# Kernel optimization log

Measured on AMD Instinct MI355X. Metric: run time of the kernel, lower is better.

## Reference

```python
import jax, jax.numpy as jnp
import numpy as np
import math

N_EMBD = 512
N_BRANCH = 4
BLOCK = 2048
B, T = 2, 2048


def make_rope_tables(dim, max_len):
    inv_freq = 1.0 / (10000.0 ** (np.arange(0, dim, 2, dtype=np.float32) / dim))
    t = np.arange(max_len, dtype=np.float32)
    freqs = np.einsum('i,j->ij', t, inv_freq)  # [max_len, dim/2]
    return jnp.asarray(np.cos(freqs)), jnp.asarray(np.sin(freqs))


def apply_rope(xq, cos, sin):
    # xq: [..., T, C]; cos/sin: [T, C/2]
    x1 = xq[..., 0::2]
    x2 = xq[..., 1::2]
    y1 = x1 * cos - x2 * sin
    y2 = x1 * sin + x2 * cos
    return jnp.stack((y1, y2), axis=-1).reshape(xq.shape)


def setup_inputs() -> dict:
    key = jax.random.key(0)
    ks = jax.random.split(key, 6)
    C, NB = N_EMBD, N_BRANCH
    s = 1.0 / math.sqrt(C)
    a = jax.random.normal(ks[0], (B, T, C), jnp.float32)
    x = jax.random.normal(ks[1], (B, T, C), jnp.float32)
    Wq = jax.random.normal(ks[2], (C, C * NB), jnp.float32) * s
    Wk = jax.random.normal(ks[3], (C, C), jnp.float32) * s
    Wv = jax.random.normal(ks[4], (C, C * NB), jnp.float32) * s
    Wo = jax.random.normal(ks[5], (C, C), jnp.float32) * s
    cos, sin = make_rope_tables(C, BLOCK)
    return {"a": a, "x": x, "Wq": Wq, "Wk": Wk, "Wv": Wv, "Wo": Wo,
            "cos": cos, "sin": sin}


def reference(a, x, Wq, Wk, Wv, Wo, cos, sin):
    Bb, Tt, C = x.shape
    NB = Wq.shape[1] // C
    cos_t = cos[:Tt]
    sin_t = sin[:Tt]

    q = (a @ Wq).reshape(Bb, Tt, NB, C).transpose(0, 2, 1, 3)  # [B,NB,T,C]
    v = (a @ Wv).reshape(Bb, Tt, NB, C).transpose(0, 2, 1, 3)  # [B,NB,T,C]
    k = (x @ Wk)[:, None, :, :]                                # [B,1,T,C]

    q = apply_rope(q, cos_t, sin_t)
    k = apply_rope(k, cos_t, sin_t)

    att = jnp.einsum('bntc,bosc->bnts', q, k) / math.sqrt(C)   # [B,NB,T,T]
    causal = jnp.tril(jnp.ones((Tt, Tt), bool))                # [T,T]
    att_m = jnp.where(causal, att, -jnp.inf)

    # softmax over branch axis; mask is identical across branches, so compute
    # on unmasked logits and zero-out masked positions (== nan_to_num of
    # softmax over fully -inf columns)
    soft_probs = jnp.where(causal, jax.nn.softmax(att, axis=1), 0.0)

    max_val = jnp.max(soft_probs, axis=1, keepdims=True)
    hard_mask = jax.lax.stop_gradient((soft_probs == max_val).astype(att.dtype))
    route_mask = jax.lax.stop_gradient(hard_mask - soft_probs) + soft_probs

    att_max = jnp.max(att_m, axis=1)                           # [B,T,T]
    attn_probs = jax.nn.softmax(att_max, axis=-1)              # [B,T,T]

    combined = attn_probs[:, None, :, :] * route_mask          # [B,NB,T,T]
    y = jnp.einsum('bnts,bnsc->btc', combined, v)              # [B,T,C]
    return y @ Wo
```

## Files before the change

### kernel.cpp

```cpp
#include <hip/hip_runtime.h>
#include <math.h>


#define B_ 2
#define T_ 2048
#define C_ 512
#define NB_ 4
#define C2_ 1024

typedef unsigned short u16;
typedef unsigned char u8;
using short8 = __attribute__((ext_vector_type(8))) short;
using bf16x8 = __attribute__((ext_vector_type(8))) __bf16;
using f32x4  = __attribute__((ext_vector_type(4))) float;

__device__ __forceinline__ float bf2f(u16 u) {
  union { unsigned int i; float f; } v; v.i = ((unsigned int)u) << 16; return v.f;
}
__device__ __forceinline__ u16 f2bf(float f) {
  union { float f; unsigned int i; } v; v.f = f;
  unsigned int u = v.i;
  return (u16)((u + 0x7fffu + ((u >> 16) & 1u)) >> 16);
}
__device__ __forceinline__ f32x4 mfma16x16x32(short8 a, short8 b, f32x4 c) {
  return __builtin_amdgcn_mfma_f32_16x16x32_bf16(
      __builtin_bit_cast(bf16x8, a), __builtin_bit_cast(bf16x8, b), c, 0, 0, 0);
}
__device__ __forceinline__ void split8(const float* s, uint4& hi, uint4& lo) {
  u16 h[8], l[8];
#pragma unroll
  for (int j = 0; j < 8; ++j) {
    h[j] = f2bf(s[j]);
    l[j] = f2bf(s[j] - bf2f(h[j]));
  }
  hi.x = h[0] | ((unsigned)h[1] << 16); hi.y = h[2] | ((unsigned)h[3] << 16);
  hi.z = h[4] | ((unsigned)h[5] << 16); hi.w = h[6] | ((unsigned)h[7] << 16);
  lo.x = l[0] | ((unsigned)l[1] << 16); lo.y = l[2] | ((unsigned)l[3] << 16);
  lo.z = l[4] | ((unsigned)l[5] << 16); lo.w = l[6] | ((unsigned)l[7] << 16);
}
__device__ __forceinline__ int swz(int row) { return ((row >> 1) & 3) << 3; }

template <int MODE>
__global__ __launch_bounds__(256) void gemm_qk(const float* __restrict__ A,
                                               const float* __restrict__ W,
                                               u16* __restrict__ out,
                                               const float* __restrict__ cosT,
                                               const float* __restrict__ sinT,
                                               const int N, const int K) {
  __shared__ u16 Ah[64][32], Al[64][32];
  __shared__ u16 Bh[64][32], Bl[64][32];
  const int tid = threadIdx.x;
  const int wave = tid >> 6, lane = tid & 63;
  const int m0 = blockIdx.y << 6, n0 = blockIdx.x << 6;
  const f32x4 zero = {0.f, 0.f, 0.f, 0.f};
  f32x4 acc[4] = {zero, zero, zero, zero};
  const int srow = tid >> 2, koff = ((tid & 3) << 3) ^ swz(tid >> 2);
  const int lrow = lane & 15, lk = ((lane >> 4) << 3) ^ swz(lane & 15);
  for (int kk = 0; kk < K; kk += 32) {
    const int kg = (tid & 3) << 3;
    float av[8];
    *(float4*)(av) = *(const float4*)(&A[(size_t)(m0 + srow) * K + kk + kg]);
    *(float4*)(av + 4) =
        *(const float4*)(&A[(size_t)(m0 + srow) * K + kk + kg + 4]);
    uint4 hi, lo;
    split8(av, hi, lo);
    *(uint4*)(&Ah[srow][koff]) = hi;
    *(uint4*)(&Al[srow][koff]) = lo;
    float wv[8];
#pragma unroll
    for (int j = 0; j < 8; ++j)
      wv[j] = W[(size_t)(kk + kg + j) * N + n0 + srow];
    split8(wv, hi, lo);
    *(uint4*)(&Bh[srow][koff]) = hi;
    *(uint4*)(&Bl[srow][koff]) = lo;
    __syncthreads();
    short8 ah = *(const short8*)(&Ah[(wave << 4) + lrow][lk]);
    short8 al = *(const short8*)(&Al[(wave << 4) + lrow][lk]);
#pragma unroll
    for (int ns = 0; ns < 4; ++ns) {
      short8 bh = *(const short8*)(&Bh[(ns << 4) + lrow][lk]);
      short8 bl = *(const short8*)(&Bl[(ns << 4) + lrow][lk]);
      acc[ns] = mfma16x16x32(ah, bh, acc[ns]);
      acc[ns] = mfma16x16x32(al, bh, acc[ns]);
      acc[ns] = mfma16x16x32(ah, bl, acc[ns]);
    }
    __syncthreads();
  }
  const int r0 = m0 + (wave << 4) + ((lane >> 4) << 2);
  const int cb = n0 + (lane & 15);
#pragma unroll
  for (int ns = 0; ns < 4; ++ns) {
#pragma unroll
    for (int r = 0; r < 4; ++r) {
      const int rg = r0 + r;
      const int cg = cb + (ns << 4);
      float v = acc[ns][r];
      float pv = __shfl_xor(v, 1);
      const int t = rg & (T_ - 1);
      const int c = (MODE == 1) ? (cg & (C_ - 1)) : cg;
      const int i = c >> 1;
      const float cf = cosT[(t << 8) + i];
      const float sf = sinT[(t << 8) + i];
      float x1 = (lane & 1) ? pv : v;
      float x2 = (lane & 1) ? v : pv;
      float y = (lane & 1) ? (x1 * sf + x2 * cf) : (x1 * cf - x2 * sf);
      if (MODE == 1) y *= 0.044194173824159216f;
      const u16 hi = f2bf(y);
      const u16 lo = f2bf(y - bf2f(hi));
      size_t rowoff;
      if (MODE == 1) {
        const int b = rg >> 11, n = cg >> 9;
        rowoff = ((size_t)((b * NB_ + n) * T_ + t)) * C2_;
      } else {
        rowoff = (size_t)rg * C2_;
      }
      out[rowoff + c] = hi;
      out[rowoff + C_ + c] = lo;
    }
  }
}

template <int AF32, int OF32>
__global__ __launch_bounds__(256) void gemm_hi(const void* __restrict__ Ap,
                                               const float* __restrict__ W,
                                               void* __restrict__ outp,
                                               const int N, const int K) {
  __shared__ u16 As[64][32];
  __shared__ u16 Bs[64][32];
  const int tid = threadIdx.x;
  const int wave = tid >> 6, lane = tid & 63;
  const int m0 = blockIdx.y << 6, n0 = blockIdx.x << 6;
  const f32x4 zero = {0.f, 0.f, 0.f, 0.f};
  f32x4 acc[4] = {zero, zero, zero, zero};
  const int srow = tid >> 2, koff = ((tid & 3) << 3) ^ swz(tid >> 2);
  const int lrow = lane & 15, lk = ((lane >> 4) << 3) ^ swz(lane & 15);
  for (int kk = 0; kk < K; kk += 32) {
    const int kg = (tid & 3) << 3;
    if (AF32) {
      const float* A = (const float*)Ap;
      float av[8];
      *(float4*)(av) = *(const float4*)(&A[(size_t)(m0 + srow) * K + kk + kg]);
      *(float4*)(av + 4) =
          *(const float4*)(&A[(size_t)(m0 + srow) * K + kk + kg + 4]);
      uint4 hi;
      hi.x = f2bf(av[0]) | ((unsigned)f2bf(av[1]) << 16);
      hi.y = f2bf(av[2]) | ((unsigned)f2bf(av[3]) << 16);
      hi.z = f2bf(av[4]) | ((unsigned)f2bf(av[5]) << 16);
      hi.w = f2bf(av[6]) | ((unsigned)f2bf(av[7]) << 16);
      *(uint4*)(&As[srow][koff]) = hi;
    } else {
      const u16* A = (const u16*)Ap;
      *(uint4*)(&As[srow][koff]) =
          *(const uint4*)(&A[(size_t)(m0 + srow) * K + kk + kg]);
    }
    uint4 hi;
    {
      float w[8];
#pragma unroll
      for (int j = 0; j < 8; ++j)
        w[j] = W[(size_t)(kk + kg + j) * N + n0 + srow];
      hi.x = f2bf(w[0]) | ((unsigned)f2bf(w[1]) << 16);
      hi.y = f2bf(w[2]) | ((unsigned)f2bf(w[3]) << 16);
      hi.z = f2bf(w[4]) | ((unsigned)f2bf(w[5]) << 16);
      hi.w = f2bf(w[6]) | ((unsigned)f2bf(w[7]) << 16);
    }
    *(uint4*)(&Bs[srow][koff]) = hi;
    __syncthreads();
    short8 af = *(const short8*)(&As[(wave << 4) + lrow][lk]);
#pragma unroll
    for (int ns = 0; ns < 4; ++ns) {
      short8 bf = *(const short8*)(&Bs[(ns << 4) + lrow][lk]);
      acc[ns] = mfma16x16x32(af, bf, acc[ns]);
    }
    __syncthreads();
  }
  const int r0 = m0 + (wave << 4) + ((lane >> 4) << 2);
  const int cb = n0 + (lane & 15);
#pragma unroll
  for (int ns = 0; ns < 4; ++ns) {
#pragma unroll
    for (int r = 0; r < 4; ++r) {
      const size_t idx = (size_t)(r0 + r) * N + cb + (ns << 4);
      if (OF32) ((float*)outp)[idx] = acc[ns][r];
      else ((u16*)outp)[idx] = f2bf(acc[ns][r]);
    }
  }
}

__global__ __launch_bounds__(256) void transpose_v_k(const u16* __restrict__ Vraw,
                                                     u16* __restrict__ VT) {
  const int bid = blockIdx.x;
  const int ct = bid & 7;
  const int ttile = (bid >> 3) & 31;
  const int n = (bid >> 8) & 3;
  const int b = bid >> 10;
  __shared__ u16 tile[64][68];
  const int tid = threadIdx.x;
  const int rr = tid >> 4;
  const int cc = (tid & 15) << 2;
  const int t0 = ttile << 6, c0 = ct << 6;
#pragma unroll
  for (int it = 0; it < 4; ++it) {
    const int r = (it << 4) + rr;
    *(ushort4*)(&tile[r][cc]) = *(const ushort4*)(
        &Vraw[((size_t)((b << 11) + t0 + r)) * (NB_ * C_) + n * C_ + c0 + cc]);
  }
  __syncthreads();
#pragma unroll
  for (int it = 0; it < 4; ++it) {
    const int c = (it << 4) + rr;
    ushort4 w;
    w.x = tile[cc + 0][c]; w.y = tile[cc + 1][c];
    w.z = tile[cc + 2][c]; w.w = tile[cc + 3][c];
    *(ushort4*)(&VT[((size_t)((b * NB_ + n) * C_ + c0 + c)) * T_ + t0 + cc]) = w;
  }
}

__global__ __launch_bounds__(256, 4) void scores_k(const u16* __restrict__ Qcat,
                                                   const u16* __restrict__ Kcat,
                                                   u16* __restrict__ Mout,
                                                   u8* __restrict__ Mask) {
  const int tri = ((blockIdx.x & 7) * 66) + (blockIdx.x >> 3);
  int tt = (int)((sqrtf(8.f * (float)tri + 1.f) - 1.f) * 0.5f);
  while ((tt + 1) * (tt + 2) / 2 <= tri) ++tt;
  while (tt * (tt + 1) / 2 > tri) --tt;
  const int ss = tri - tt * (tt + 1) / 2;
  const int b = blockIdx.y;
  __shared__ __align__(16) u16 Kh[2][64][32], Kl[2][64][32];
  const int tid = threadIdx.x;
  const int wave = tid >> 6, lane = tid & 63;
  const int t0 = tt << 6, s0 = ss << 6;
  const f32x4 zero = {0.f, 0.f, 0.f, 0.f};
  f32x4 acc[NB_][4];
  for (int n = 0; n < NB_; ++n)
    for (int j = 0; j < 4; ++j) acc[n][j] = zero;
  const int srow = tid >> 2, kg = (tid & 3) << 3;
  const int lrow = lane & 15, lk = (lane >> 4) << 3;
  const int wrow = wave << 4;
  const size_t qstride = (size_t)T_ * C2_;
  const size_t qb0 =
      ((size_t)(b * NB_ * T_ + t0 + wrow + lrow)) * C2_ + lk;
  const size_t kbase = ((size_t)((b << 11) + s0 + srow)) * C2_ + kg;

  auto stage_k = [&](int d, int kko) {
    __builtin_amdgcn_global_load_lds(
        (const __attribute__((address_space(1))) void*)&Kcat[kbase + kko],
        (__attribute__((address_space(3))) void*)&Kh[d][wrow][0], 16, 0, 0);
    __builtin_amdgcn_global_load_lds(
        (const __attribute__((address_space(1))) void*)&Kcat[kbase + kko + C_],
        (__attribute__((address_space(3))) void*)&Kl[d][wrow][0], 16, 0, 0);
  };

  stage_k(0, 0);
  int cur = 0;
  for (int kk = 0; kk < C_; kk += 32) {
    if (kk + 32 < C_) stage_k(cur ^ 1, kk + 32);
    short8 qh[NB_], ql[NB_];
#pragma unroll
    for (int n = 0; n < NB_; ++n) {
      const size_t qb = qb0 + (size_t)n * qstride + kk;
      qh[n] = *(const short8*)(&Qcat[qb]);
      ql[n] = *(const short8*)(&Qcat[qb + C_]);
    }
    if (kk + 32 < C_) {
      asm volatile("s_waitcnt vmcnt(2)" ::: "memory");
    } else {
      asm volatile("s_waitcnt vmcnt(0)" ::: "memory");
    }
    __builtin_amdgcn_sched_barrier(0);
    __builtin_amdgcn_s_barrier();
    __builtin_amdgcn_sched_barrier(0);
#pragma unroll
    for (int ns = 0; ns < 4; ++ns) {
      short8 kh = *(const short8*)(&Kh[cur][(ns << 4) + lrow][lk]);
      short8 kl = *(const short8*)(&Kl[cur][(ns << 4) + lrow][lk]);
#pragma unroll
      for (int n = 0; n < NB_; ++n) {
        acc[n][ns] = mfma16x16x32(qh[n], kh, acc[n][ns]);
        acc[n][ns] = mfma16x16x32(ql[n], kh, acc[n][ns]);
        acc[n][ns] = mfma16x16x32(qh[n], kl, acc[n][ns]);
      }
    }
    __builtin_amdgcn_sched_barrier(0);
    asm volatile("" ::: "memory");
    __builtin_amdgcn_s_barrier();
    __builtin_amdgcn_sched_barrier(0);
    cur ^= 1;
  }
  const int tb = t0 + (wave << 4) + ((lane >> 4) << 2);
  const int sb = s0 + (lane & 15);
#pragma unroll
  for (int ns = 0; ns < 4; ++ns) {
#pragma unroll
    for (int r = 0; r < 4; ++r) {
      const int t = tb + r, s = sb + (ns << 4);
      float a0 = acc[0][ns][r], a1 = acc[1][ns][r];
      float a2 = acc[2][ns][r], a3 = acc[3][ns][r];
      float m = fmaxf(fmaxf(a0, a1), fmaxf(a2, a3));
      u8 msk = (u8)((a0 == m) | ((a1 == m) << 1) | ((a2 == m) << 2) |
                    ((a3 == m) << 3));
      if (s > t) { m = -__builtin_inff(); msk = 0; }
      const size_t idx = (size_t)b * T_ * T_ + (size_t)t * T_ + s;
      Mout[idx] = f2bf(m);
      Mask[idx] = msk;
    }
  }
}

__global__ __launch_bounds__(256) void rowstats_k(const u16* __restrict__ Mb,
                                                  float* __restrict__ Rm,
                                                  float* __restrict__ Rz) {
  const int r = (blockIdx.x << 2) + (threadIdx.x >> 6);
  const int lane = threadIdx.x & 63;
  const int b = r >> 11, t = r & (T_ - 1);
  const u16* row = Mb + (size_t)b * T_ * T_ + (size_t)t * T_;
  float m = -__builtin_inff();
  for (int s = lane; s <= t; s += 64) m = fmaxf(m, bf2f(row[s]));
#pragma unroll
  for (int off = 32; off; off >>= 1) m = fmaxf(m, __shfl_xor(m, off));
  float z = 0.f;
  for (int s = lane; s <= t; s += 64) z += expf(bf2f(row[s]) - m);
#pragma unroll
  for (int off = 32; off; off >>= 1) z += __shfl_xor(z, off);
  if (lane == 0) { Rm[r] = m; Rz[r] = 1.f / z; }
}

__global__ __launch_bounds__(256) void pbuild_k(const u16* __restrict__ Mb,
                                                const float* __restrict__ Rm,
                                                const float* __restrict__ Rz,
                                                u16* __restrict__ Pb) {
  const int r = blockIdx.x;
  const float rm = Rm[r], rz = Rz[r];
  const size_t off = ((size_t)r << 11) + (threadIdx.x << 3);
  ushort4 m0 = *(const ushort4*)(&Mb[off]);
  ushort4 m1 = *(const ushort4*)(&Mb[off + 4]);
  u16 o[8];
  o[0] = f2bf(expf(bf2f(m0.x) - rm) * rz);
  o[1] = f2bf(expf(bf2f(m0.y) - rm) * rz);
  o[2] = f2bf(expf(bf2f(m0.z) - rm) * rz);
  o[3] = f2bf(expf(bf2f(m0.w) - rm) * rz);
  o[4] = f2bf(expf(bf2f(m1.x) - rm) * rz);
  o[5] = f2bf(expf(bf2f(m1.y) - rm) * rz);
  o[6] = f2bf(expf(bf2f(m1.z) - rm) * rz);
  o[7] = f2bf(expf(bf2f(m1.w) - rm) * rz);
  uint4 w;
  w.x = o[0] | ((unsigned)o[1] << 16); w.y = o[2] | ((unsigned)o[3] << 16);
  w.z = o[4] | ((unsigned)o[5] << 16); w.w = o[6] | ((unsigned)o[7] << 16);
  *(uint4*)(&Pb[off]) = w;
}

__global__ __launch_bounds__(256) void pv_k(const u16* __restrict__ Pb,
                                            const u8* __restrict__ Mask,
                                            const u16* __restrict__ VT,
                                            u16* __restrict__ Y) {
  const int ypair = blockIdx.x, cblk = blockIdx.y, b = blockIdx.z;
  const int c0 = cblk << 5;
  __shared__ u16 Ps[NB_][64][32];
  __shared__ u16 Vs[NB_][32][32];
  const int tid = threadIdx.x;
  const int wave = tid >> 6, lane = tid & 63;
  const int prow = tid >> 2, soff = (tid & 3) << 3;
  const int psoff = soff ^ swz(prow);
  const int vrow = tid >> 3, vsoff = (tid & 7) << 2;
  const int vcol = ((((tid & 7) >> 1) ^ ((vrow >> 1) & 3)) << 3) |
                   ((tid & 1) << 2);
  const int lrow = lane & 15, lk = ((lane >> 4) << 3) ^ swz(lane & 15);
  const f32x4 zero = {0.f, 0.f, 0.f, 0.f};
  const size_t vrow_base[NB_] = {
      ((size_t)((b * NB_ + 0) * C_ + c0 + vrow)) * T_,
      ((size_t)((b * NB_ + 1) * C_ + c0 + vrow)) * T_,
      ((size_t)((b * NB_ + 2) * C_ + c0 + vrow)) * T_,
      ((size_t)((b * NB_ + 3) * C_ + c0 + vrow)) * T_};

  for (int half = 0; half < 2; ++half) {
    const int tt = half ? (31 - ypair) : ypair;
    const int t0 = tt << 6;
    const int nchunk = (tt + 1) << 1;
    const size_t pro = ((size_t)((b << 11) + t0 + prow)) << 11;
    f32x4 acc[2] = {zero, zero};
    uint4 pu; uint2 mk2; uint2 vv[NB_];
    pu = *(const uint4*)(&Pb[pro + soff]);
    mk2 = *(const uint2*)(&Mask[pro + soff]);
#pragma unroll
    for (int n = 0; n < NB_; ++n)
      vv[n] = *(const uint2*)(&VT[vrow_base[n] + vsoff]);
    for (int ck = 0; ck < nchunk; ++ck) {
      u16 p[8] = {(u16)pu.x, (u16)(pu.x >> 16), (u16)pu.y, (u16)(pu.y >> 16),
                  (u16)pu.z, (u16)(pu.z >> 16), (u16)pu.w, (u16)(pu.w >> 16)};
      u8 mk[8] = {(u8)mk2.x, (u8)(mk2.x >> 8), (u8)(mk2.x >> 16),
                  (u8)(mk2.x >> 24), (u8)mk2.y, (u8)(mk2.y >> 8),
                  (u8)(mk2.y >> 16), (u8)(mk2.y >> 24)};
#pragma unroll
      for (int n = 0; n < NB_; ++n) {
        uint4 wv;
        wv.x = (unsigned)(((mk[0] >> n) & 1) ? p[0] : 0) |
               ((unsigned)(((mk[1] >> n) & 1) ? p[1] : 0) << 16);
        wv.y = (unsigned)(((mk[2] >> n) & 1) ? p[2] : 0) |
               ((unsigned)(((mk[3] >> n) & 1) ? p[3] : 0) << 16);
        wv.z = (unsigned)(((mk[4] >> n) & 1) ? p[4] : 0) |
               ((unsigned)(((mk[5] >> n) & 1) ? p[5] : 0) << 16);
        wv.w = (unsigned)(((mk[6] >> n) & 1) ? p[6] : 0) |
               ((unsigned)(((mk[7] >> n) & 1) ? p[7] : 0) << 16);
        *(uint4*)(&Ps[n][prow][psoff]) = wv;
        *(uint2*)(&Vs[n][vrow][vcol]) = vv[n];
      }
      __syncthreads();
      if (ck + 1 < nchunk) {
        const int sB = (ck + 1) << 5;
        pu = *(const uint4*)(&Pb[pro + sB + soff]);
        mk2 = *(const uint2*)(&Mask[pro + sB + soff]);
#pragma unroll
        for (int n = 0; n < NB_; ++n)
          vv[n] = *(const uint2*)(&VT[vrow_base[n] + sB + vsoff]);
      }
#pragma unroll
      for (int n = 0; n < NB_; ++n) {
        short8 af = *(const short8*)(&Ps[n][(wave << 4) + lrow][lk]);
#pragma unroll
        for (int cs = 0; cs < 2; ++cs) {
          short8 bf = *(const short8*)(&Vs[n][(cs << 4) + lrow][lk]);
          acc[cs] = mfma16x16x32(af, bf, acc[cs]);
        }
      }
      __syncthreads();
    }
    const int tb = t0 + (wave << 4) + ((lane >> 4) << 2);
    const int cbs = c0 + (lane & 15);
#pragma unroll
    for (int cs = 0; cs < 2; ++cs) {
#pragma unroll
      for (int r = 0; r < 4; ++r) {
        Y[(size_t)((b << 11) + tb + r) * C_ + cbs + (cs << 4)] =
            f2bf(acc[cs][r]);
      }
    }
  }
}

extern "C" void kernel_launch(void* const* d_in, const int* in_sizes, int n_in,
                              void* d_out, int out_size, void* d_ws,
                              size_t ws_size, hipStream_t stream) {
  (void)in_sizes; (void)n_in; (void)out_size; (void)ws_size;
  const float* a    = (const float*)d_in[0];
  const float* x    = (const float*)d_in[1];
  const float* Wq   = (const float*)d_in[2];
  const float* Wk   = (const float*)d_in[3];
  const float* Wv   = (const float*)d_in[4];
  const float* Wo   = (const float*)d_in[5];
  const float* cosT = (const float*)d_in[6];
  const float* sinT = (const float*)d_in[7];

  char* w = (char*)d_ws;
  u16* Qcat   = (u16*)(w + 0);
  u16* Kcat   = (u16*)(w + 33554432);
  u16* Vraw   = (u16*)(w + 41943040);
  u16* VT     = (u16*)(w + 58720256);
  u8*  Mask   = (u8*)(w + 75497472);
  float* Rm   = (float*)(w + 83886080);
  float* Rz   = (float*)(w + 83902464);
  u16* Pb     = (u16*)(w + 83918848);
  u16* Mb     = Vraw;
  u16* Y      = Qcat;

  const dim3 blk(256);
  gemm_qk<1><<<dim3(32, 64), blk, 0, stream>>>(a, Wq, Qcat, cosT, sinT, 2048, 512);
  gemm_qk<2><<<dim3(8, 64), blk, 0, stream>>>(x, Wk, Kcat, cosT, sinT, 512, 512);
  gemm_hi<1, 0><<<dim3(32, 64), blk, 0, stream>>>(a, Wv, (void*)Vraw, 2048, 512);
  transpose_v_k<<<dim3(2048), blk, 0, stream>>>(Vraw, VT);
  scores_k<<<dim3(528, 2), blk, 0, stream>>>(Qcat, Kcat, Mb, Mask);
  rowstats_k<<<dim3(1024), blk, 0, stream>>>(Mb, Rm, Rz);
  pbuild_k<<<dim3(4096), blk, 0, stream>>>(Mb, Rm, Rz, Pb);
  pv_k<<<dim3(16, 16, 2), blk, 0, stream>>>(Pb, Mask, VT, Y);
  gemm_hi<0, 1><<<dim3(8, 64), blk, 0, stream>>>(Y, Wo, d_out, 512, 512);
}
```

Baseline: 392.8 us.

## Double-buffer Q register loads alongside K staging in scores kernel

Unrolls the K-loop of the scores kernel by two and double-buffers the Q fragments in registers, so the next step's Q global loads are issued before the current step's MFMAs, as the K LDS stages already were. It also raises wave priority around the MFMA block and relaxes the launch-bounds occupancy hint from 4 to 3 blocks per CU to leave room for the extra registers. This is meant to hide Q global-load latency. The cost is higher register pressure and possibly lower occupancy.

```diff
diff --git a/kernel.cpp b/kernel.cpp
--- a/kernel.cpp
+++ b/kernel.cpp
@@ -216,7 +216,7 @@
   }
 }
 
-__global__ __launch_bounds__(256, 4) void scores_k(const u16* __restrict__ Qcat,
+__global__ __launch_bounds__(256, 3) void scores_k(const u16* __restrict__ Qcat,
                                                    const u16* __restrict__ Kcat,
                                                    u16* __restrict__ Mout,
                                                    u8* __restrict__ Mask) {
@@ -250,30 +250,20 @@
         (const __attribute__((address_space(1))) void*)&Kcat[kbase + kko + C_],
         (__attribute__((address_space(3))) void*)&Kl[d][wrow][0], 16, 0, 0);
   };
-
-  stage_k(0, 0);
-  int cur = 0;
-  for (int kk = 0; kk < C_; kk += 32) {
-    if (kk + 32 < C_) stage_k(cur ^ 1, kk + 32);
-    short8 qh[NB_], ql[NB_];
+  auto loadQ = [&](int kko, short8* qh, short8* ql) {
 #pragma unroll
     for (int n = 0; n < NB_; ++n) {
-      const size_t qb = qb0 + (size_t)n * qstride + kk;
+      const size_t qb = qb0 + (size_t)n * qstride + kko;
       qh[n] = *(const short8*)(&Qcat[qb]);
       ql[n] = *(const short8*)(&Qcat[qb + C_]);
     }
-    if (kk + 32 < C_) {
-      asm volatile("s_waitcnt vmcnt(2)" ::: "memory");
-    } else {
-      asm volatile("s_waitcnt vmcnt(0)" ::: "memory");
-    }
-    __builtin_amdgcn_sched_barrier(0);
-    __builtin_amdgcn_s_barrier();
-    __builtin_amdgcn_sched_barrier(0);
+  };
+  auto mma = [&](const short8* qh, const short8* ql, int d) {
+    __builtin_amdgcn_s_setprio(1);
 #pragma unroll
     for (int ns = 0; ns < 4; ++ns) {
-      short8 kh = *(const short8*)(&Kh[cur][(ns << 4) + lrow][lk]);
-      short8 kl = *(const short8*)(&Kl[cur][(ns << 4) + lrow][lk]);
+      short8 kh = *(const short8*)(&Kh[d][(ns << 4) + lrow][lk]);
+      short8 kl = *(const short8*)(&Kl[d][(ns << 4) + lrow][lk]);
 #pragma unroll
       for (int n = 0; n < NB_; ++n) {
         acc[n][ns] = mfma16x16x32(qh[n], kh, acc[n][ns]);
@@ -281,11 +271,39 @@
         acc[n][ns] = mfma16x16x32(qh[n], kl, acc[n][ns]);
       }
     }
+    __builtin_amdgcn_s_setprio(0);
+  };
+
+  short8 qhA[NB_], qlA[NB_], qhB[NB_], qlB[NB_];
+  loadQ(0, qhA, qlA);
+  stage_k(0, 0);
+  for (int k = 0; k < C_; k += 64) {
+    stage_k(1, k + 32);
+    loadQ(k + 32, qhB, qlB);
+    asm volatile("s_waitcnt vmcnt(10)" ::: "memory");
+    __builtin_amdgcn_sched_barrier(0);
+    __builtin_amdgcn_s_barrier();
+    __builtin_amdgcn_sched_barrier(0);
+    mma(qhA, qlA, 0);
     __builtin_amdgcn_sched_barrier(0);
     asm volatile("" ::: "memory");
     __builtin_amdgcn_s_barrier();
     __builtin_amdgcn_sched_barrier(0);
-    cur ^= 1;
+    if (k + 64 < C_) {
+      stage_k(0, k + 64);
+      loadQ(k + 64, qhA, qlA);
+      asm volatile("s_waitcnt vmcnt(10)" ::: "memory");
+    } else {
+      asm volatile("s_waitcnt vmcnt(0)" ::: "memory");
+    }
+    __builtin_amdgcn_sched_barrier(0);
+    __builtin_amdgcn_s_barrier();
+    __builtin_amdgcn_sched_barrier(0);
+    mma(qhB, qlB, 1);
+    __builtin_amdgcn_sched_barrier(0);
+    asm volatile("" ::: "memory");
+    __builtin_amdgcn_s_barrier();
+    __builtin_amdgcn_sched_barrier(0);
   }
   const int tb = t0 + (wave << 4) + ((lane >> 4) << 2);
   const int sb = s0 + (lane & 15);
```

Measured after the change: 392.5 us. Within noise of the previous version (-0.1%).
